# Optimization experiments

Measured on AMD Instinct MI355X. Metric: run time of the kernel, lower is better.

## Reference

```python
import jax, jax.numpy as jnp
import numpy as np
from jax import lax

# BatchNorm2d(affine=False) in eval mode with initial running stats (mean=0, var=1)
# reduces to a constant scale. (Original torch module in train mode would use batch
# stats of the dispatched subset; we use the eval-mode form for a deterministic,
# vectorizable reference.)
BN_SCALE = 1.0 / np.sqrt(1.0 + 1e-5)
DN = ('NCHW', 'OIHW', 'NCHW')


def _dw(x, w, pad, dil=1):
    # depthwise conv, kernel [C,1,k,k]
    return lax.conv_general_dilated(x, w, (1, 1), [(pad, pad), (pad, pad)],
                                    rhs_dilation=(dil, dil), dimension_numbers=DN,
                                    feature_group_count=x.shape[1])


def _pw(x, w):
    # pointwise 1x1 conv, kernel [C,C,1,1]
    return lax.conv_general_dilated(x, w, (1, 1), 'VALID', dimension_numbers=DN)


def _sep(x, d1, p1, d2, p2, pad):
    # DARTS SepConv: (ReLU-dw-pw-BN) x 2
    y = _pw(_dw(jax.nn.relu(x), d1, pad), p1) * BN_SCALE
    return _pw(_dw(jax.nn.relu(y), d2, pad), p2) * BN_SCALE


def _dil(x, d, p, pad):
    # DARTS DilConv: ReLU-dw(dilation=2)-pw-BN
    return _pw(_dw(jax.nn.relu(x), d, pad, 2), p) * BN_SCALE


def _maxpool3(x):
    y = jnp.pad(x, ((0, 0), (0, 0), (1, 1), (1, 1)), constant_values=-jnp.inf)
    return lax.reduce_window(y, -jnp.inf, lax.max, (1, 1, 3, 3), (1, 1, 1, 1), 'VALID')


def _avgpool3(x):
    # avg_pool 3x3 stride 1 pad 1, count_include_pad=False
    pad = [(0, 0), (0, 0), (1, 1), (1, 1)]
    s = lax.reduce_window(x, 0.0, lax.add, (1, 1, 3, 3), (1, 1, 1, 1), pad)
    c = lax.reduce_window(jnp.ones_like(x), 0.0, lax.add, (1, 1, 3, 3), (1, 1, 1, 1), pad)
    return s / c


def _mixed_forward(x, weights, params, top):
    B, n_op = weights.shape
    _, idx = lax.top_k(weights, top)                    # [B, top]
    sel = jax.nn.one_hot(idx, n_op).sum(axis=1) > 0     # [B, n_op] bool: op in top-k
    # softmax over logits masked to -inf outside top-k => non-selected ops weight 0
    gate = jax.nn.softmax(jnp.where(sel, weights, -jnp.inf), axis=-1)  # [B, n_op]
    (sc3_d1, sc3_p1, sc3_d2, sc3_p2,
     sc5_d1, sc5_p1, sc5_d2, sc5_p2,
     dc3_d, dc3_p, dc5_d, dc5_p) = params
    # PRIMITIVES order: none, max_pool_3x3, avg_pool_3x3, skip_connect,
    # sep_conv_3x3, sep_conv_5x5, dil_conv_3x3, dil_conv_5x5
    op_outs = [
        None,                        # 'none' contributes zeros
        _maxpool3(x) * BN_SCALE,     # pool ops are followed by BN(affine=False)
        _avgpool3(x) * BN_SCALE,
        x,                           # skip_connect (stride=1 -> Identity)
        _sep(x, sc3_d1, sc3_p1, sc3_d2, sc3_p2, 1),
        _sep(x, sc5_d1, sc5_p1, sc5_d2, sc5_p2, 2),
        _dil(x, dc3_d, dc3_p, 2),
        _dil(x, dc5_d, dc5_p, 4),
    ]
    out = jnp.zeros_like(x)
    for i, y in enumerate(op_outs):
        if y is not None:
            out = out + gate[:, i, None, None, None] * y
    return out, weights  # second output is gate_value_cp (clone of gate input)


def setup_inputs():
    key = jax.random.key(0)
    ks = jax.random.split(key, 16)
    B, C, H, W = 64, 128, 32, 32
    def p(k, shape):
        return jax.random.normal(k, shape, jnp.float32) * 0.05
    return {
        'x': jax.random.normal(ks[0], (B, C, H, W), jnp.float32),
        'weights': jax.random.normal(ks[1], (B, 8), jnp.float32),
        'sc3_d1': p(ks[2], (C, 1, 3, 3)), 'sc3_p1': p(ks[3], (C, C, 1, 1)),
        'sc3_d2': p(ks[4], (C, 1, 3, 3)), 'sc3_p2': p(ks[5], (C, C, 1, 1)),
        'sc5_d1': p(ks[6], (C, 1, 5, 5)), 'sc5_p1': p(ks[7], (C, C, 1, 1)),
        'sc5_d2': p(ks[8], (C, 1, 5, 5)), 'sc5_p2': p(ks[9], (C, C, 1, 1)),
        'dc3_d': p(ks[10], (C, 1, 3, 3)), 'dc3_p': p(ks[11], (C, C, 1, 1)),
        'dc5_d': p(ks[12], (C, 1, 5, 5)), 'dc5_p': p(ks[13], (C, C, 1, 1)),
        'top': 2,
    }


def reference(x, weights, sc3_d1, sc3_p1, sc3_d2, sc3_p2, sc5_d1, sc5_p1, sc5_d2, sc5_p2, dc3_d, dc3_p, dc5_d, dc5_p, top):
    params = (sc3_d1, sc3_p1, sc3_d2, sc3_p2, sc5_d1, sc5_p1, sc5_d2, sc5_p2,
              dc3_d, dc3_p, dc5_d, dc5_p)
    return _mixed_forward(x, weights, params, top)
```

## Files before the change

kernel.cpp:

```cpp
#include <hip/hip_runtime.h>
#include <hip/hip_bf16.h>


#define BN_SCALE 0.9999950000374997f
#define BB 64
#define CC 128
#define HH 32
#define WW 32
#define PLANE (HH*WW)
#define SAMP (CC*PLANE)
#define NOUT0 (BB*SAMP)

typedef __attribute__((ext_vector_type(8))) short bf16x8;
typedef __attribute__((ext_vector_type(4))) float f32x4;

__device__ __forceinline__ float us2f(unsigned int u) {
    unsigned int x = (u & 0xffffu) << 16;
    float f; __builtin_memcpy(&f, &x, 4); return f;
}
__device__ __forceinline__ unsigned short f2us(float f) {
    __hip_bfloat16 h = __float2bfloat16(f);
    unsigned short u; __builtin_memcpy(&u, &h, 2); return u;
}

__global__ __launch_bounds__(256) void
k_gates_prep(const float* __restrict__ wlog,
             const void* __restrict__ topp,
             const float* __restrict__ w0, const float* __restrict__ w1,
             const float* __restrict__ w2, const float* __restrict__ w3,
             const float* __restrict__ w4, const float* __restrict__ w5,
             float* __restrict__ gates,
             int* __restrict__ cnum, int* __restrict__ cops,
             float* __restrict__ out_w,
             unsigned short* __restrict__ Wbf) {
    if (blockIdx.x != 0) {
        int idx = (blockIdx.x - 1) * 256 + threadIdx.x;
        int mat = idx >> 14, e = idx & 16383;
        const float* src; float s = 1.f;
        switch (mat) {
            case 0:  src = w0; s = BN_SCALE; break;
            case 1:  src = w1; s = BN_SCALE; break;
            case 2:  src = w2; break;
            case 3:  src = w3; break;
            case 4:  src = w4; break;
            default: src = w5; break;
        }
        Wbf[idx] = f2us(src[e] * s);
        return;
    }
    if (threadIdx.x >= BB) return;
    int b = threadIdx.x;

    int top = -1;
    {
        unsigned int u0 = *(const unsigned int*)topp;
        int i32 = (int)u0;
        if (i32 >= 1 && i32 <= 8) top = i32;
        else {
            float f32; __builtin_memcpy(&f32, &u0, 4);
            if (f32 >= 1.f && f32 <= 8.f) top = (int)(f32 + 0.5f);
            else { float fb = us2f(u0); if (fb >= 1.f && fb <= 8.f) top = (int)(fb + 0.5f); }
        }
        if (top < 1 || top > 8) top = 2;
    }

    float lw[8];
    #pragma unroll
    for (int i = 0; i < 8; ++i) {
        lw[i] = wlog[b * 8 + i];
        out_w[b * 8 + i] = lw[i];
    }
    bool sel[8] = {false,false,false,false,false,false,false,false};
    for (int t = 0; t < top; ++t) {
        int best = -1; float bv = -3.4e38f;
        #pragma unroll
        for (int i = 0; i < 8; ++i)
            if (!sel[i] && lw[i] > bv) { bv = lw[i]; best = i; }
        if (best >= 0) sel[best] = true;
    }
    float m = -3.4e38f;
    #pragma unroll
    for (int i = 0; i < 8; ++i) if (sel[i] && lw[i] > m) m = lw[i];
    float s = 0.f, e[8];
    #pragma unroll
    for (int i = 0; i < 8; ++i) { e[i] = sel[i] ? expf(lw[i] - m) : 0.f; s += e[i]; }
    float inv = (s > 0.f) ? 1.f / s : 0.f;
    float g[8];
    #pragma unroll
    for (int i = 0; i < 8; ++i) {
        g[i] = (s > 0.f) ? e[i] * inv : (sel[i] ? 1.f / (float)top : 0.f);
        gates[b * 8 + i] = g[i];
    }
    int n = 0;
    #pragma unroll
    for (int i = 4; i < 8; ++i)
        if (g[i] > 0.f) { if (n < 4) cops[b * 4 + n] = i; ++n; }
    cnum[b] = (n < 4) ? n : 4;
}

template <int K, int DIL>
__device__ __forceinline__ void dw_comp(const float* __restrict__ sx,
                                        const float* __restrict__ wd, int c,
                                        unsigned short* __restrict__ opp) {
    constexpr int PAD = (K / 2) * DIL;
    float wk[K * K];
    #pragma unroll
    for (int i = 0; i < K * K; ++i) wk[i] = wd[c * K * K + i];
    #pragma unroll
    for (int j = 0; j < 4; ++j) {
        int px = threadIdx.x + j * 256;
        int h = px >> 5, w = px & 31;
        float acc = 0.f;
        #pragma unroll
        for (int ky = 0; ky < K; ++ky) {
            int ih = h + ky * DIL - PAD;
            if ((unsigned)ih >= HH) continue;
            #pragma unroll
            for (int kx = 0; kx < K; ++kx) {
                int iw = w + kx * DIL - PAD;
                if ((unsigned)iw >= WW) continue;
                acc = fmaf(wk[ky * K + kx], sx[ih * WW + iw], acc);
            }
        }
        opp[px] = f2us(acc);
    }
}

__global__ __launch_bounds__(256) void
k_front(const float* __restrict__ x,
        const float* __restrict__ w4, const float* __restrict__ w5,
        const float* __restrict__ w6, const float* __restrict__ w7,
        const float* __restrict__ gates,
        float* __restrict__ out,
        unsigned short* __restrict__ A4, unsigned short* __restrict__ A5,
        unsigned short* __restrict__ P6, unsigned short* __restrict__ P7) {
    int plane = blockIdx.x;
    int b = plane >> 7, c = plane & 127;
    float g1 = gates[b * 8 + 1] * BN_SCALE;
    float g2 = gates[b * 8 + 2] * BN_SCALE;
    float g3 = gates[b * 8 + 3];
    float g4 = gates[b * 8 + 4], g5 = gates[b * 8 + 5];
    float g6 = gates[b * 8 + 6], g7 = gates[b * 8 + 7];
    bool haspool = (g1 != 0.f) | (g2 != 0.f) | (g3 != 0.f);
    bool hasdw   = (g4 != 0.f) | (g5 != 0.f) | (g6 != 0.f) | (g7 != 0.f);
    float* op = out + (size_t)plane * PLANE;
    if (!haspool && !hasdw) {
        ((float4*)op)[threadIdx.x] = make_float4(0.f, 0.f, 0.f, 0.f);
        return;
    }
    __shared__ float sxr[PLANE];
    __shared__ float sxf[PLANE];
    {
        float4 v = ((const float4*)(x + (size_t)plane * PLANE))[threadIdx.x];
        ((float4*)sxr)[threadIdx.x] = v;
        ((float4*)sxf)[threadIdx.x] =
            make_float4(fmaxf(v.x, 0.f), fmaxf(v.y, 0.f),
                        fmaxf(v.z, 0.f), fmaxf(v.w, 0.f));
    }
    __syncthreads();

    if (haspool) {
        #pragma unroll
        for (int j = 0; j < 4; ++j) {
            int px = threadIdx.x + j * 256;
            int h = px >> 5, w = px & 31;
            float mx = -3.4e38f, sm = 0.f;
            int cnt = 0;
            #pragma unroll
            for (int dh = -1; dh <= 1; ++dh) {
                int ih = h + dh;
                if ((unsigned)ih >= HH) continue;
                #pragma unroll
                for (int dw = -1; dw <= 1; ++dw) {
                    int iw = w + dw;
                    if ((unsigned)iw >= WW) continue;
                    float v = sxr[ih * WW + iw];
                    mx = fmaxf(mx, v);
                    sm += v;
                    ++cnt;
                }
            }
            op[px] = g1 * mx + g2 * (sm / (float)cnt) + g3 * sxr[px];
        }
    } else {
        ((float4*)op)[threadIdx.x] = make_float4(0.f, 0.f, 0.f, 0.f);
    }

    size_t off = (size_t)plane * PLANE;
    if (g4 != 0.f) dw_comp<3, 1>(sxf, w4, c, A4 + off);
    if (g5 != 0.f) dw_comp<5, 1>(sxf, w5, c, A5 + off);
    if (g6 != 0.f) dw_comp<3, 2>(sxf, w6, c, P6 + off);
    if (g7 != 0.f) dw_comp<5, 2>(sxf, w7, c, P7 + off);
}

__global__ __launch_bounds__(256) void
k_dw_second(const unsigned short* __restrict__ B4,
            const unsigned short* __restrict__ B5,
            const float* __restrict__ w4, const float* __restrict__ w5,
            const float* __restrict__ gates,
            unsigned short* __restrict__ P4, unsigned short* __restrict__ P5) {
    int plane = blockIdx.x;
    int b = plane >> 7, c = plane & 127;
    float g4 = gates[b * 8 + 4], g5 = gates[b * 8 + 5];
    if (g4 == 0.f && g5 == 0.f) return;
    __shared__ float sx[PLANE];
    size_t off = (size_t)plane * PLANE;
    if (g4 != 0.f) {
        ushort4 v = ((const ushort4*)(B4 + off))[threadIdx.x];
        ((float4*)sx)[threadIdx.x] =
            make_float4(fmaxf(us2f(v.x), 0.f), fmaxf(us2f(v.y), 0.f),
                        fmaxf(us2f(v.z), 0.f), fmaxf(us2f(v.w), 0.f));
        __syncthreads();
        dw_comp<3, 1>(sx, w4, c, P4 + off);
        __syncthreads();
    }
    if (g5 != 0.f) {
        ushort4 v = ((const ushort4*)(B5 + off))[threadIdx.x];
        ((float4*)sx)[threadIdx.x] =
            make_float4(fmaxf(us2f(v.x), 0.f), fmaxf(us2f(v.y), 0.f),
                        fmaxf(us2f(v.z), 0.f), fmaxf(us2f(v.w), 0.f));
        __syncthreads();
        dw_comp<5, 1>(sx, w5, c, P5 + off);
    }
}


__device__ __forceinline__ void stage_bt(unsigned int* __restrict__ BtU,
                                         const unsigned short* __restrict__ A,
                                         int hw0, float s) {
    unsigned short* Bs = (unsigned short*)BtU;
    #pragma unroll
    for (int i = 0; i < 16; ++i) {
        int idx = threadIdx.x + i * 256;
        int ci = idx >> 5, p = idx & 31;
        unsigned int raw = *(const unsigned int*)(A + (size_t)ci * PLANE + hw0 + 2 * p);
        Bs[(2 * p) * 130 + ci]     = f2us(us2f(raw) * s);
        Bs[(2 * p + 1) * 130 + ci] = f2us(us2f(raw >> 16) * s);
    }
}

__device__ __forceinline__ bf16x8 afrag(const unsigned int* __restrict__ BtU,
                                        int r, int ko2) {
    union { unsigned int u[4]; bf16x8 v; } f;
    #pragma unroll
    for (int j = 0; j < 4; ++j) f.u[j] = BtU[r * 65 + ko2 + j];
    return f.v;
}

__global__ __launch_bounds__(256) void
k_pw_mid(const unsigned short* __restrict__ A4,
         const unsigned short* __restrict__ A5,
         const unsigned short* __restrict__ Wbf,
         const float* __restrict__ gates,
         unsigned short* __restrict__ B4, unsigned short* __restrict__ B5) {
    int blk = blockIdx.x;
    int hwt = blk & 15;
    int opi = (blk >> 4) & 1;
    int b = blk >> 5;
    if (gates[b * 8 + 4 + opi] == 0.f) return;
    int hw0 = hwt * 64;
    int wave = threadIdx.x >> 6, lane = threadIdx.x & 63;
    int q = lane >> 4, mm = lane & 15;
    int r = wave * 16 + mm;
    __shared__ unsigned int BtU[64 * 65];
    stage_bt(BtU, (opi ? A5 : A4) + (size_t)b * SAMP, hw0, 1.f);
    __syncthreads();
    const unsigned short* Wb = Wbf + opi * 16384;
    f32x4 acc[8];
    #pragma unroll
    for (int i = 0; i < 8; ++i) acc[i] = (f32x4){0.f, 0.f, 0.f, 0.f};
    #pragma unroll
    for (int kb = 0; kb < 4; ++kb) {
        bf16x8 a = afrag(BtU, r, kb * 16 + q * 4);
        #pragma unroll
        for (int nt = 0; nt < 8; ++nt) {
            bf16x8 bv = *(const bf16x8*)(Wb + (nt * 16 + mm) * CC + kb * 32 + q * 8);
            acc[nt] = __builtin_amdgcn_mfma_f32_16x16x32_bf16(a, bv, acc[nt], 0, 0, 0);
        }
    }
    unsigned short* ob = (opi ? B5 : B4) + (size_t)b * SAMP;
    int hwbase = hw0 + wave * 16 + q * 4;
    #pragma unroll
    for (int nt = 0; nt < 8; ++nt) {
        int co = nt * 16 + mm;
        uint2 pk;
        pk.x = (unsigned int)f2us(acc[nt][0]) | ((unsigned int)f2us(acc[nt][1]) << 16);
        pk.y = (unsigned int)f2us(acc[nt][2]) | ((unsigned int)f2us(acc[nt][3]) << 16);
        *(uint2*)(ob + (size_t)co * PLANE + hwbase) = pk;
    }
}

__global__ __launch_bounds__(256) void
k_pw_final(const unsigned short* __restrict__ P4,
           const unsigned short* __restrict__ P5,
           const unsigned short* __restrict__ P6,
           const unsigned short* __restrict__ P7,
           const unsigned short* __restrict__ Wbf,
           const float* __restrict__ gates,
           const int* __restrict__ cnum, const int* __restrict__ cops,
           float* __restrict__ out) {
    int blk = blockIdx.x;
    int hwt = blk & 15;
    int b = blk >> 4;
    int n = cnum[b];
    if (n == 0) return;
    int hw0 = hwt * 64;
    int wave = threadIdx.x >> 6, lane = threadIdx.x & 63;
    int q = lane >> 4, mm = lane & 15;
    int r = wave * 16 + mm;
    __shared__ unsigned int BtU[64 * 65];
    f32x4 acc[8];
    #pragma unroll
    for (int i = 0; i < 8; ++i) acc[i] = (f32x4){0.f, 0.f, 0.f, 0.f};
    for (int t = 0; t < n; ++t) {
        int op = cops[b * 4 + t];
        float gs = gates[b * 8 + op] * BN_SCALE;
        const unsigned short* src;
        switch (op) {
            case 4:  src = P4; break;
            case 5:  src = P5; break;
            case 6:  src = P6; break;
            default: src = P7; break;
        }
        if (t) __syncthreads();
        stage_bt(BtU, src + (size_t)b * SAMP, hw0, gs);
        __syncthreads();
        const unsigned short* Wb = Wbf + (op - 2) * 16384;
        #pragma unroll
        for (int kb = 0; kb < 4; ++kb) {
            bf16x8 a = afrag(BtU, r, kb * 16 + q * 4);
            #pragma unroll
            for (int nt = 0; nt < 8; ++nt) {
                bf16x8 bv = *(const bf16x8*)(Wb + (nt * 16 + mm) * CC + kb * 32 + q * 8);
                acc[nt] = __builtin_amdgcn_mfma_f32_16x16x32_bf16(a, bv, acc[nt], 0, 0, 0);
            }
        }
    }
    int hwbase = hw0 + wave * 16 + q * 4;
    #pragma unroll
    for (int nt = 0; nt < 8; ++nt) {
        int co = nt * 16 + mm;
        float* p = out + (size_t)(b * CC + co) * PLANE + hwbase;
        float4 o = *(float4*)p;
        o.x += acc[nt][0]; o.y += acc[nt][1];
        o.z += acc[nt][2]; o.w += acc[nt][3];
        *(float4*)p = o;
    }
}

extern "C" void kernel_launch(void* const* d_in, const int* in_sizes, int n_in,
                              void* d_out, int out_size, void* d_ws, size_t ws_size,
                              hipStream_t stream) {
    const float* x      = (const float*)d_in[0];
    const float* wlog   = (const float*)d_in[1];
    const float* sc3_d1 = (const float*)d_in[2];
    const float* sc3_p1 = (const float*)d_in[3];
    const float* sc3_d2 = (const float*)d_in[4];
    const float* sc3_p2 = (const float*)d_in[5];
    const float* sc5_d1 = (const float*)d_in[6];
    const float* sc5_p1 = (const float*)d_in[7];
    const float* sc5_d2 = (const float*)d_in[8];
    const float* sc5_p2 = (const float*)d_in[9];
    const float* dc3_d  = (const float*)d_in[10];
    const float* dc3_p  = (const float*)d_in[11];
    const float* dc5_d  = (const float*)d_in[12];
    const float* dc5_p  = (const float*)d_in[13];
    const void* topp    = d_in[14];

    float* out  = (float*)d_out;
    float* outw = out + NOUT0;

    float* gates = (float*)d_ws;
    int*   cnum  = (int*)((char*)d_ws + 2048);
    int*   cops  = (int*)((char*)d_ws + 2304);
    unsigned short* Wbf  = (unsigned short*)((char*)d_ws + 4096);
    unsigned short* base = (unsigned short*)((char*)d_ws + 200704);
    unsigned short* A4 = base;
    unsigned short* A5 = base + (size_t)NOUT0;
    unsigned short* B4 = base + (size_t)NOUT0 * 2;
    unsigned short* B5 = base + (size_t)NOUT0 * 3;
    unsigned short* P4 = base + (size_t)NOUT0 * 4;
    unsigned short* P5 = base + (size_t)NOUT0 * 5;
    unsigned short* P6 = base + (size_t)NOUT0 * 6;
    unsigned short* P7 = base + (size_t)NOUT0 * 7;

    k_gates_prep<<<385, 256, 0, stream>>>(wlog, topp,
                                          sc3_p1, sc5_p1, sc3_p2, sc5_p2,
                                          dc3_p, dc5_p,
                                          gates, cnum, cops, outw, Wbf);
    k_front<<<BB * CC, 256, 0, stream>>>(x, sc3_d1, sc5_d1, dc3_d, dc5_d,
                                         gates, out, A4, A5, P6, P7);
    k_pw_mid<<<BB * 32, 256, 0, stream>>>(A4, A5, Wbf, gates, B4, B5);
    k_dw_second<<<BB * CC, 256, 0, stream>>>(B4, B5, sc3_d2, sc5_d2, gates, P4, P5);
    k_pw_final<<<BB * 16, 256, 0, stream>>>(P4, P5, P6, P7, Wbf,
                                            gates, cnum, cops, out);
}
```

Before: 193.9 us.

## Fuse gate prep into front kernel and sep-conv mid stages into tail

Gate computation and weight conversion move into extra blocks of the front kernel, and each plane block recomputes its gates locally, which removes one launch. The sep-conv middle pointwise GEMM, ReLU and second depthwise conv are fused into the final pointwise kernel. Each tile recomputes halo rows through the mid GEMM and keeps them in LDS, which removes two launches and the B/P intermediate round trips to global memory. The cost is redundant halo compute, higher LDS use and per-block register pressure, which limits occupancy in the tail kernel.

```diff
diff --git a/kernel.cpp b/kernel.cpp
--- a/kernel.cpp
+++ b/kernel.cpp
@@ -23,53 +23,24 @@
     unsigned short u; __builtin_memcpy(&u, &h, 2); return u;
 }
 
-__global__ __launch_bounds__(256) void
-k_gates_prep(const float* __restrict__ wlog,
-             const void* __restrict__ topp,
-             const float* __restrict__ w0, const float* __restrict__ w1,
-             const float* __restrict__ w2, const float* __restrict__ w3,
-             const float* __restrict__ w4, const float* __restrict__ w5,
-             float* __restrict__ gates,
-             int* __restrict__ cnum, int* __restrict__ cops,
-             float* __restrict__ out_w,
-             unsigned short* __restrict__ Wbf) {
-    if (blockIdx.x != 0) {
-        int idx = (blockIdx.x - 1) * 256 + threadIdx.x;
-        int mat = idx >> 14, e = idx & 16383;
-        const float* src; float s = 1.f;
-        switch (mat) {
-            case 0:  src = w0; s = BN_SCALE; break;
-            case 1:  src = w1; s = BN_SCALE; break;
-            case 2:  src = w2; break;
-            case 3:  src = w3; break;
-            case 4:  src = w4; break;
-            default: src = w5; break;
-        }
-        Wbf[idx] = f2us(src[e] * s);
-        return;
-    }
-    if (threadIdx.x >= BB) return;
-    int b = threadIdx.x;
-
+__device__ __forceinline__ void compute_gates(const float* __restrict__ wlog,
+                                              const void* __restrict__ topp,
+                                              int b, float* g) {
     int top = -1;
     {
         unsigned int u0 = *(const unsigned int*)topp;
         int i32 = (int)u0;
         if (i32 >= 1 && i32 <= 8) top = i32;
         else {
-            float f32; __builtin_memcpy(&f32, &u0, 4);
-            if (f32 >= 1.f && f32 <= 8.f) top = (int)(f32 + 0.5f);
+            float f32v; __builtin_memcpy(&f32v, &u0, 4);
+            if (f32v >= 1.f && f32v <= 8.f) top = (int)(f32v + 0.5f);
             else { float fb = us2f(u0); if (fb >= 1.f && fb <= 8.f) top = (int)(fb + 0.5f); }
         }
         if (top < 1 || top > 8) top = 2;
     }
-
     float lw[8];
     #pragma unroll
-    for (int i = 0; i < 8; ++i) {
-        lw[i] = wlog[b * 8 + i];
-        out_w[b * 8 + i] = lw[i];
-    }
+    for (int i = 0; i < 8; ++i) lw[i] = wlog[b * 8 + i];
     bool sel[8] = {false,false,false,false,false,false,false,false};
     for (int t = 0; t < top; ++t) {
         int best = -1; float bv = -3.4e38f;
@@ -85,17 +56,9 @@
     #pragma unroll
     for (int i = 0; i < 8; ++i) { e[i] = sel[i] ? expf(lw[i] - m) : 0.f; s += e[i]; }
     float inv = (s > 0.f) ? 1.f / s : 0.f;
-    float g[8];
-    #pragma unroll
-    for (int i = 0; i < 8; ++i) {
+    #pragma unroll
+    for (int i = 0; i < 8; ++i)
         g[i] = (s > 0.f) ? e[i] * inv : (sel[i] ? 1.f / (float)top : 0.f);
-        gates[b * 8 + i] = g[i];
-    }
-    int n = 0;
-    #pragma unroll
-    for (int i = 4; i < 8; ++i)
-        if (g[i] > 0.f) { if (n < 4) cops[b * 4 + n] = i; ++n; }
-    cnum[b] = (n < 4) ? n : 4;
 }
 
 template <int K, int DIL>
@@ -127,20 +90,60 @@
 }
 
 __global__ __launch_bounds__(256) void
-k_front(const float* __restrict__ x,
-        const float* __restrict__ w4, const float* __restrict__ w5,
-        const float* __restrict__ w6, const float* __restrict__ w7,
-        const float* __restrict__ gates,
-        float* __restrict__ out,
-        unsigned short* __restrict__ A4, unsigned short* __restrict__ A5,
-        unsigned short* __restrict__ P6, unsigned short* __restrict__ P7) {
+k_front_all(const float* __restrict__ x,
+            const float* __restrict__ w4, const float* __restrict__ w5,
+            const float* __restrict__ w6, const float* __restrict__ w7,
+            const float* __restrict__ wlog, const void* __restrict__ topp,
+            const float* __restrict__ pw0, const float* __restrict__ pw1,
+            const float* __restrict__ pw2, const float* __restrict__ pw3,
+            const float* __restrict__ pw4, const float* __restrict__ pw5,
+            float* __restrict__ gates,
+            int* __restrict__ cnum, int* __restrict__ cops,
+            float* __restrict__ out_w,
+            unsigned short* __restrict__ Wbf,
+            float* __restrict__ out,
+            unsigned short* __restrict__ A4, unsigned short* __restrict__ A5,
+            unsigned short* __restrict__ P6, unsigned short* __restrict__ P7) {
+    if (blockIdx.x >= BB * CC) {
+        int aux = blockIdx.x - BB * CC;
+        if (aux < 384) {
+            int idx = aux * 256 + threadIdx.x;
+            int mat = idx >> 14, e = idx & 16383;
+            const float* src; float s = 1.f;
+            switch (mat) {
+                case 0:  src = pw0; s = BN_SCALE; break;
+                case 1:  src = pw1; s = BN_SCALE; break;
+                case 2:  src = pw2; break;
+                case 3:  src = pw3; break;
+                case 4:  src = pw4; break;
+                default: src = pw5; break;
+            }
+            Wbf[idx] = f2us(src[e] * s);
+        } else if (threadIdx.x < BB) {
+            int b = threadIdx.x;
+            float g[8];
+            compute_gates(wlog, topp, b, g);
+            #pragma unroll
+            for (int i = 0; i < 8; ++i) {
+                out_w[b * 8 + i] = wlog[b * 8 + i];
+                gates[b * 8 + i] = g[i];
+            }
+            int n = 0;
+            #pragma unroll
+            for (int i = 4; i < 8; ++i)
+                if (g[i] > 0.f) { if (n < 4) cops[b * 4 + n] = i; ++n; }
+            cnum[b] = (n < 4) ? n : 4;
+        }
+        return;
+    }
     int plane = blockIdx.x;
     int b = plane >> 7, c = plane & 127;
-    float g1 = gates[b * 8 + 1] * BN_SCALE;
-    float g2 = gates[b * 8 + 2] * BN_SCALE;
-    float g3 = gates[b * 8 + 3];
-    float g4 = gates[b * 8 + 4], g5 = gates[b * 8 + 5];
-    float g6 = gates[b * 8 + 6], g7 = gates[b * 8 + 7];
+    float g[8];
+    compute_gates(wlog, topp, b, g);
+    float g1 = g[1] * BN_SCALE;
+    float g2 = g[2] * BN_SCALE;
+    float g3 = g[3];
+    float g4 = g[4], g5 = g[5], g6 = g[6], g7 = g[7];
     bool haspool = (g1 != 0.f) | (g2 != 0.f) | (g3 != 0.f);
     bool hasdw   = (g4 != 0.f) | (g5 != 0.f) | (g6 != 0.f) | (g7 != 0.f);
     float* op = out + (size_t)plane * PLANE;
@@ -193,37 +196,6 @@
     if (g7 != 0.f) dw_comp<5, 2>(sxf, w7, c, P7 + off);
 }
 
-__global__ __launch_bounds__(256) void
-k_dw_second(const unsigned short* __restrict__ B4,
-            const unsigned short* __restrict__ B5,
-            const float* __restrict__ w4, const float* __restrict__ w5,
-            const float* __restrict__ gates,
-            unsigned short* __restrict__ P4, unsigned short* __restrict__ P5) {
-    int plane = blockIdx.x;
-    int b = plane >> 7, c = plane & 127;
-    float g4 = gates[b * 8 + 4], g5 = gates[b * 8 + 5];
-    if (g4 == 0.f && g5 == 0.f) return;
-    __shared__ float sx[PLANE];
-    size_t off = (size_t)plane * PLANE;
-    if (g4 != 0.f) {
-        ushort4 v = ((const ushort4*)(B4 + off))[threadIdx.x];
-        ((float4*)sx)[threadIdx.x] =
-            make_float4(fmaxf(us2f(v.x), 0.f), fmaxf(us2f(v.y), 0.f),
-                        fmaxf(us2f(v.z), 0.f), fmaxf(us2f(v.w), 0.f));
-        __syncthreads();
-        dw_comp<3, 1>(sx, w4, c, P4 + off);
-        __syncthreads();
-    }
-    if (g5 != 0.f) {
-        ushort4 v = ((const ushort4*)(B5 + off))[threadIdx.x];
-        ((float4*)sx)[threadIdx.x] =
-            make_float4(fmaxf(us2f(v.x), 0.f), fmaxf(us2f(v.y), 0.f),
-                        fmaxf(us2f(v.z), 0.f), fmaxf(us2f(v.w), 0.f));
-        __syncthreads();
-        dw_comp<5, 1>(sx, w5, c, P5 + off);
-    }
-}
-
 
 __device__ __forceinline__ void stage_bt(unsigned int* __restrict__ BtU,
                                          const unsigned short* __restrict__ A,
@@ -239,6 +211,23 @@
     }
 }
 
+__device__ __forceinline__ void stage_bt_z(unsigned int* __restrict__ BtU,
+                                           const unsigned short* __restrict__ A,
+                                           int hw0) {
+    unsigned short* Bs = (unsigned short*)BtU;
+    #pragma unroll
+    for (int i = 0; i < 16; ++i) {
+        int idx = threadIdx.x + i * 256;
+        int ci = idx >> 5, p = idx & 31;
+        int pg = hw0 + 2 * p;
+        unsigned int raw = 0u;
+        if ((unsigned)pg < (unsigned)PLANE)
+            raw = *(const unsigned int*)(A + (size_t)ci * PLANE + pg);
+        Bs[(2 * p) * 130 + ci]     = (unsigned short)(raw & 0xffffu);
+        Bs[(2 * p + 1) * 130 + ci] = (unsigned short)(raw >> 16);
+    }
+}
+
 __device__ __forceinline__ bf16x8 afrag(const unsigned int* __restrict__ BtU,
                                         int r, int ko2) {
     union { unsigned int u[4]; bf16x8 v; } f;
@@ -247,58 +236,95 @@
     return f.v;
 }
 
-__global__ __launch_bounds__(256) void
-k_pw_mid(const unsigned short* __restrict__ A4,
-         const unsigned short* __restrict__ A5,
-         const unsigned short* __restrict__ Wbf,
-         const float* __restrict__ gates,
-         unsigned short* __restrict__ B4, unsigned short* __restrict__ B5) {
-    int blk = blockIdx.x;
-    int hwt = blk & 15;
-    int opi = (blk >> 4) & 1;
-    int b = blk >> 5;
-    if (gates[b * 8 + 4 + opi] == 0.f) return;
-    int hw0 = hwt * 64;
+template <int K>
+__device__ __forceinline__ void
+sep_to_bt(unsigned int* __restrict__ BtU, unsigned short* __restrict__ Braw,
+          const unsigned short* __restrict__ Asrc,
+          const unsigned short* __restrict__ Wmid,
+          const float* __restrict__ wd, int hwt, float gs) {
+    constexpr int PAD = K / 2, NR = K + 1, NSEG = NR / 2, S = 196;
     int wave = threadIdx.x >> 6, lane = threadIdx.x & 63;
     int q = lane >> 4, mm = lane & 15;
     int r = wave * 16 + mm;
-    __shared__ unsigned int BtU[64 * 65];
-    stage_bt(BtU, (opi ? A5 : A4) + (size_t)b * SAMP, hw0, 1.f);
+    int rbase = 2 * hwt - PAD;
+    for (int seg = 0; seg < NSEG; ++seg) {
+        if (seg) __syncthreads();
+        stage_bt_z(BtU, Asrc, rbase * 32 + seg * 64);
+        __syncthreads();
+        f32x4 accB[8];
+        #pragma unroll
+        for (int i = 0; i < 8; ++i) accB[i] = (f32x4){0.f, 0.f, 0.f, 0.f};
+        #pragma unroll
+        for (int kb = 0; kb < 4; ++kb) {
+            bf16x8 a = afrag(BtU, r, kb * 16 + q * 4);
+            #pragma unroll
+            for (int nt = 0; nt < 8; ++nt) {
+                bf16x8 bv = *(const bf16x8*)(Wmid + (nt * 16 + mm) * CC + kb * 32 + q * 8);
+                accB[nt] = __builtin_amdgcn_mfma_f32_16x16x32_bf16(a, bv, accB[nt], 0, 0, 0);
+            }
+        }
+        int pxb = seg * 64 + wave * 16 + q * 4;
+        #pragma unroll
+        for (int nt = 0; nt < 8; ++nt) {
+            int co = nt * 16 + mm;
+            ushort4 v;
+            v.x = f2us(fmaxf(accB[nt][0], 0.f));
+            v.y = f2us(fmaxf(accB[nt][1], 0.f));
+            v.z = f2us(fmaxf(accB[nt][2], 0.f));
+            v.w = f2us(fmaxf(accB[nt][3], 0.f));
+            *(ushort4*)(Braw + (size_t)co * S + pxb) = v;
+        }
+    }
     __syncthreads();
-    const unsigned short* Wb = Wbf + opi * 16384;
-    f32x4 acc[8];
-    #pragma unroll
-    for (int i = 0; i < 8; ++i) acc[i] = (f32x4){0.f, 0.f, 0.f, 0.f};
-    #pragma unroll
-    for (int kb = 0; kb < 4; ++kb) {
-        bf16x8 a = afrag(BtU, r, kb * 16 + q * 4);
-        #pragma unroll
-        for (int nt = 0; nt < 8; ++nt) {
-            bf16x8 bv = *(const bf16x8*)(Wb + (nt * 16 + mm) * CC + kb * 32 + q * 8);
-            acc[nt] = __builtin_amdgcn_mfma_f32_16x16x32_bf16(a, bv, acc[nt], 0, 0, 0);
-        }
-    }
-    unsigned short* ob = (opi ? B5 : B4) + (size_t)b * SAMP;
-    int hwbase = hw0 + wave * 16 + q * 4;
-    #pragma unroll
-    for (int nt = 0; nt < 8; ++nt) {
-        int co = nt * 16 + mm;
-        uint2 pk;
-        pk.x = (unsigned int)f2us(acc[nt][0]) | ((unsigned int)f2us(acc[nt][1]) << 16);
-        pk.y = (unsigned int)f2us(acc[nt][2]) | ((unsigned int)f2us(acc[nt][3]) << 16);
-        *(uint2*)(ob + (size_t)co * PLANE + hwbase) = pk;
-    }
-}
-
-__global__ __launch_bounds__(256) void
-k_pw_final(const unsigned short* __restrict__ P4,
-           const unsigned short* __restrict__ P5,
-           const unsigned short* __restrict__ P6,
-           const unsigned short* __restrict__ P7,
-           const unsigned short* __restrict__ Wbf,
-           const float* __restrict__ gates,
-           const int* __restrict__ cnum, const int* __restrict__ cops,
-           float* __restrict__ out) {
+
+    int ci = threadIdx.x & 127, h = threadIdx.x >> 7;
+    float wk[K * K];
+    #pragma unroll
+    for (int i = 0; i < K * K; ++i) wk[i] = wd[ci * K * K + i];
+    float acc[32];
+    #pragma unroll
+    for (int w = 0; w < 32; ++w) acc[w] = 0.f;
+    const unsigned short* rowp = Braw + (size_t)ci * S + h * 32;
+    #pragma unroll
+    for (int ky = 0; ky < K; ++ky) {
+        float win[40];
+        #pragma unroll
+        for (int k = 0; k < 10; ++k) {
+            if (k == 0 || k == 9) {
+                win[4*k] = win[4*k+1] = win[4*k+2] = win[4*k+3] = 0.f;
+            } else {
+                ushort4 v = *(const ushort4*)(rowp + ky * 32 + (k - 1) * 4);
+                win[4*k]   = us2f(v.x);
+                win[4*k+1] = us2f(v.y);
+                win[4*k+2] = us2f(v.z);
+                win[4*k+3] = us2f(v.w);
+            }
+        }
+        #pragma unroll
+        for (int kx = 0; kx < K; ++kx) {
+            float f = wk[ky * K + kx];
+            #pragma unroll
+            for (int w = 0; w < 32; ++w)
+                acc[w] = fmaf(f, win[w + kx - PAD + 4], acc[w]);
+        }
+    }
+    unsigned short* Bs = (unsigned short*)BtU;
+    #pragma unroll
+    for (int w = 0; w < 32; ++w)
+        Bs[(h * 32 + w) * 130 + ci] = f2us(acc[w] * gs);
+    __syncthreads();
+}
+
+__global__ __launch_bounds__(256, 2) void
+k_tail(const unsigned short* __restrict__ A4,
+       const unsigned short* __restrict__ A5,
+       const unsigned short* __restrict__ P6,
+       const unsigned short* __restrict__ P7,
+       const unsigned short* __restrict__ Wbf,
+       const float* __restrict__ gates,
+       const int* __restrict__ cnum, const int* __restrict__ cops,
+       const float* __restrict__ wd3, const float* __restrict__ wd5,
+       float* __restrict__ out) {
     int blk = blockIdx.x;
     int hwt = blk & 15;
     int b = blk >> 4;
@@ -309,22 +335,22 @@
     int q = lane >> 4, mm = lane & 15;
     int r = wave * 16 + mm;
     __shared__ unsigned int BtU[64 * 65];
+    __shared__ unsigned short Braw[128 * 196];
     f32x4 acc[8];
     #pragma unroll
     for (int i = 0; i < 8; ++i) acc[i] = (f32x4){0.f, 0.f, 0.f, 0.f};
     for (int t = 0; t < n; ++t) {
         int op = cops[b * 4 + t];
         float gs = gates[b * 8 + op] * BN_SCALE;
-        const unsigned short* src;
-        switch (op) {
-            case 4:  src = P4; break;
-            case 5:  src = P5; break;
-            case 6:  src = P6; break;
-            default: src = P7; break;
-        }
         if (t) __syncthreads();
-        stage_bt(BtU, src + (size_t)b * SAMP, hw0, gs);
-        __syncthreads();
+        if (op >= 6) {
+            stage_bt(BtU, (op == 6 ? P6 : P7) + (size_t)b * SAMP, hw0, gs);
+            __syncthreads();
+        } else if (op == 4) {
+            sep_to_bt<3>(BtU, Braw, A4 + (size_t)b * SAMP, Wbf, wd3, hwt, gs);
+        } else {
+            sep_to_bt<5>(BtU, Braw, A5 + (size_t)b * SAMP, Wbf + 16384, wd5, hwt, gs);
+        }
         const unsigned short* Wb = Wbf + (op - 2) * 16384;
         #pragma unroll
         for (int kb = 0; kb < 4; ++kb) {
@@ -377,21 +403,16 @@
     unsigned short* base = (unsigned short*)((char*)d_ws + 200704);
     unsigned short* A4 = base;
     unsigned short* A5 = base + (size_t)NOUT0;
-    unsigned short* B4 = base + (size_t)NOUT0 * 2;
-    unsigned short* B5 = base + (size_t)NOUT0 * 3;
-    unsigned short* P4 = base + (size_t)NOUT0 * 4;
-    unsigned short* P5 = base + (size_t)NOUT0 * 5;
-    unsigned short* P6 = base + (size_t)NOUT0 * 6;
-    unsigned short* P7 = base + (size_t)NOUT0 * 7;
-
-    k_gates_prep<<<385, 256, 0, stream>>>(wlog, topp,
-                                          sc3_p1, sc5_p1, sc3_p2, sc5_p2,
-                                          dc3_p, dc5_p,
-                                          gates, cnum, cops, outw, Wbf);
-    k_front<<<BB * CC, 256, 0, stream>>>(x, sc3_d1, sc5_d1, dc3_d, dc5_d,
-                                         gates, out, A4, A5, P6, P7);
-    k_pw_mid<<<BB * 32, 256, 0, stream>>>(A4, A5, Wbf, gates, B4, B5);
-    k_dw_second<<<BB * CC, 256, 0, stream>>>(B4, B5, sc3_d2, sc5_d2, gates, P4, P5);
-    k_pw_final<<<BB * 16, 256, 0, stream>>>(P4, P5, P6, P7, Wbf,
-                                            gates, cnum, cops, out);
-}
+    unsigned short* P6 = base + (size_t)NOUT0 * 2;
+    unsigned short* P7 = base + (size_t)NOUT0 * 3;
+
+    k_front_all<<<BB * CC + 385, 256, 0, stream>>>(
+        x, sc3_d1, sc5_d1, dc3_d, dc5_d,
+        wlog, topp,
+        sc3_p1, sc5_p1, sc3_p2, sc5_p2, dc3_p, dc5_p,
+        gates, cnum, cops, outw, Wbf,
+        out, A4, A5, P6, P7);
+    k_tail<<<BB * 16, 256, 0, stream>>>(A4, A5, P6, P7, Wbf,
+                                        gates, cnum, cops,
+                                        sc3_d2, sc5_d2, out);
+}
```

After: 269.1 us. 1.39x slower.
